# Optimization experiments

Hardware: AMD Instinct MI355X
Metric: run time of the kernel (lower is better)

## Reference

```python
import jax, jax.numpy as jnp
import numpy as np

N = 100000
E = 3200000
IN_C = 128
HID = [32, 32]
OUT_C = 32
NEG_SLOPE = 0.2  # PyG GATConv default leaky_relu slope


def setup_inputs() -> dict:
    key = jax.random.key(0)
    ks = jax.random.split(key, 16)
    x = jax.random.normal(ks[0], (N, IN_C), dtype=jnp.float32)
    edge_index = jax.random.randint(ks[1], (2, E), 0, N, dtype=jnp.int32)

    def glorot(k, shape):
        fan_in, fan_out = shape[0], shape[-1]
        lim = jnp.sqrt(6.0 / (fan_in + fan_out))
        return jax.random.uniform(k, shape, jnp.float32, -lim, lim)

    # GAT layer 1: 128 -> 32, heads=1
    W1 = glorot(ks[2], (IN_C, HID[0]))
    a_src1 = glorot(ks[3], (HID[0],))
    a_dst1 = glorot(ks[4], (HID[0],))
    b1 = jnp.zeros((HID[0],), jnp.float32)
    # GAT layer 2: 32 -> 32
    W2 = glorot(ks[5], (HID[0], HID[1]))
    a_src2 = glorot(ks[6], (HID[1],))
    a_dst2 = glorot(ks[7], (HID[1],))
    b2 = jnp.zeros((HID[1],), jnp.float32)
    # classifier: 32 -> 32
    Wc = glorot(ks[8], (HID[1], OUT_C))
    bc = jnp.zeros((OUT_C,), jnp.float32)
    return {"x": x, "edge_index": edge_index,
            "W1": W1, "a_src1": a_src1, "a_dst1": a_dst1, "b1": b1,
            "W2": W2, "a_src2": a_src2, "a_dst2": a_dst2, "b2": b2,
            "Wc": Wc, "bc": bc}


def gat_conv(h_in, src, dst, W, a_src, a_dst, b, n_nodes):
    """PyG GATConv with heads=1: linear, per-edge leaky-relu score,
    segment-softmax over incoming edges of dst, weighted scatter-sum."""
    h = h_in @ W                                   # [N, C]
    s_src = h @ a_src                              # [N]
    s_dst = h @ a_dst                              # [N]
    e = jax.nn.leaky_relu(s_src[src] + s_dst[dst], NEG_SLOPE)  # [E']
    m = jax.ops.segment_max(e, dst, num_segments=n_nodes)
    m = jnp.where(jnp.isfinite(m), m, 0.0)
    ex = jnp.exp(e - m[dst])
    z = jax.ops.segment_sum(ex, dst, num_segments=n_nodes)
    alpha = ex / (z[dst] + 1e-16)                  # [E']
    out = jax.ops.segment_sum(alpha[:, None] * h[src], dst, num_segments=n_nodes)
    return out + b


def reference(x, edge_index, W1, a_src1, a_dst1, b1, W2, a_src2, a_dst2, b2, Wc, bc):
    n = x.shape[0]
    # PyG GATConv default add_self_loops=True
    loop = jnp.arange(n, dtype=edge_index.dtype)
    src = jnp.concatenate([edge_index[0], loop])
    dst = jnp.concatenate([edge_index[1], loop])
    h = jax.nn.relu(gat_conv(x, src, dst, W1, a_src1, a_dst1, b1, n))
    h = jax.nn.relu(gat_conv(h, src, dst, W2, a_src2, a_dst2, b2, n))
    logits = h @ Wc + bc
    return jax.nn.sigmoid(logits)
```

## Files before the change

kernel.cpp:

```cpp
#include <hip/hip_runtime.h>
#include <hip/hip_fp16.h>
#include <math.h>

#define NS 0.2f

__device__ __forceinline__ float lrelu(float x) { return fmaxf(x, NS * x); }


__global__ __launch_bounds__(256) void k_feat1(
    const float* __restrict__ X, const float* __restrict__ W,
    const float* __restrict__ a_s, const float* __restrict__ a_d,
    __half* __restrict__ H, float* __restrict__ Ss, float* __restrict__ Sd, int n)
{
    __shared__ float Wl[128 * 32];
    __shared__ float Xl[8 * 128];
    const int tid = threadIdx.x;
    for (int i = tid; i < 128 * 32; i += 256) Wl[i] = W[i];

    const int row0 = blockIdx.x * 8;
    {
        int idx = tid * 4;
        int r = idx >> 7, c = idx & 127;
        if (row0 + r < n)
            *reinterpret_cast<float4*>(&Xl[idx]) =
                *reinterpret_cast<const float4*>(&X[(size_t)(row0 + r) * 128 + c]);
    }
    __syncthreads();

    const int r = tid >> 5, c = tid & 31;
    const int row = row0 + r;
    if (row >= n) return;

    float acc = 0.f;
#pragma unroll
    for (int k = 0; k < 128; ++k) acc += Xl[r * 128 + k] * Wl[k * 32 + c];
    H[(size_t)row * 32 + c] = __float2half(acc);

    float vs = acc * a_s[c];
    float vd = acc * a_d[c];
#pragma unroll
    for (int o = 16; o; o >>= 1) { vs += __shfl_xor(vs, o, 32); vd += __shfl_xor(vd, o, 32); }
    if (c == 0) { Ss[row] = vs; Sd[row] = vd; }
}

__global__ __launch_bounds__(256) void k_feat2(
    const float* __restrict__ In, const float* __restrict__ W,
    const float* __restrict__ bias,
    const float* __restrict__ a_s, const float* __restrict__ a_d,
    __half* __restrict__ H, float* __restrict__ Ss, float* __restrict__ Sd, int n)
{
    __shared__ float Wl[32 * 32];
    __shared__ float Xl[8 * 32];
    const int tid = threadIdx.x;
    for (int i = tid; i < 1024; i += 256) Wl[i] = W[i];

    const int r = tid >> 5, c = tid & 31;
    const int row = blockIdx.x * 8 + r;
    if (row < n) Xl[tid] = fmaxf(In[(size_t)row * 32 + c] + bias[c], 0.f);
    __syncthreads();
    if (row >= n) return;

    float acc = 0.f;
#pragma unroll
    for (int k = 0; k < 32; ++k) acc += Xl[r * 32 + k] * Wl[k * 32 + c];
    H[(size_t)row * 32 + c] = __float2half(acc);

    float vs = acc * a_s[c];
    float vd = acc * a_d[c];
#pragma unroll
    for (int o = 16; o; o >>= 1) { vs += __shfl_xor(vs, o, 32); vd += __shfl_xor(vd, o, 32); }
    if (c == 0) { Ss[row] = vs; Sd[row] = vd; }
}

__global__ __launch_bounds__(256) void k_cls(
    const float* __restrict__ In, const float* __restrict__ W,
    const float* __restrict__ b_prev, const float* __restrict__ bc,
    float* __restrict__ Out, int n)
{
    __shared__ float Wl[32 * 32];
    __shared__ float Xl[8 * 32];
    const int tid = threadIdx.x;
    for (int i = tid; i < 1024; i += 256) Wl[i] = W[i];

    const int r = tid >> 5, c = tid & 31;
    const int row = blockIdx.x * 8 + r;
    if (row < n) Xl[tid] = fmaxf(In[(size_t)row * 32 + c] + b_prev[c], 0.f);
    __syncthreads();
    if (row >= n) return;

    float acc = bc[c];
#pragma unroll
    for (int k = 0; k < 32; ++k) acc += Xl[r * 32 + k] * Wl[k * 32 + c];
    Out[(size_t)row * 32 + c] = 1.f / (1.f + __expf(-acc));
}


#define NBH 256

__global__ __launch_bounds__(256) void k_bhist(const int* __restrict__ edst, int E,
                                               int* __restrict__ hpart, int ngroups)
{
    __shared__ int h[512];
    const int tid = threadIdx.x;
    for (int i = tid; i < ngroups; i += 256) h[i] = 0;
    __syncthreads();
    const int nv = E >> 2;
    for (int i = blockIdx.x * 256 + tid; i < nv; i += NBH * 256) {
        int4 d = *reinterpret_cast<const int4*>(&edst[i << 2]);
        atomicAdd(&h[d.x >> 8], 1); atomicAdd(&h[d.y >> 8], 1);
        atomicAdd(&h[d.z >> 8], 1); atomicAdd(&h[d.w >> 8], 1);
    }
    if (blockIdx.x == 0 && tid < (E & 3))
        atomicAdd(&h[edst[(nv << 2) + tid] >> 8], 1);
    __syncthreads();
    for (int i = tid; i < ngroups; i += 256) hpart[i * NBH + blockIdx.x] = h[i];
}

__global__ __launch_bounds__(512) void k_bscan(const int* __restrict__ hpart, int ngroups,
    int* __restrict__ bstart, int* __restrict__ bcur, int* __restrict__ off,
    int N, int E)
{
    __shared__ int sm[512];
    int t = threadIdx.x;
    int v = 0;
    if (t < ngroups) {
        const int4* row = reinterpret_cast<const int4*>(&hpart[t * NBH]);
#pragma unroll 4
        for (int b = 0; b < NBH / 4; ++b) { int4 x = row[b]; v += x.x + x.y + x.z + x.w; }
    }
    sm[t] = v; __syncthreads();
    for (int o = 1; o < 512; o <<= 1) {
        int x = sm[t];
        if (t >= o) x += sm[t - o];
        __syncthreads();
        sm[t] = x;
        __syncthreads();
    }
    if (t <= ngroups) {
        int ex = (t == 0) ? 0 : sm[t - 1];
        bstart[t] = ex;
        if (t < ngroups) bcur[t] = ex;
    }
    if (t == 0) off[N] = E + N;
}

#define CHUNK 4096
#define KPT 16

__global__ __launch_bounds__(256) void k_part(
    const int* __restrict__ esrc, const int* __restrict__ edst, int E,
    int* __restrict__ bcur, unsigned int* __restrict__ ebuf, int ngroups)
{
    __shared__ int hist[512];
    __shared__ int lofs[513];
    __shared__ int gbase[512];
    __shared__ unsigned int stage[CHUNK];
    __shared__ unsigned short bstage[CHUNK];
    const int tid = threadIdx.x;

    for (int c0 = blockIdx.x * CHUNK; c0 < E; c0 += gridDim.x * CHUNK) {
        const int cnt = min(CHUNK, E - c0);
        for (int i = tid; i < 512; i += 256) hist[i] = 0;
        __syncthreads();

        int bp[KPT];
#pragma unroll
        for (int k = 0; k < KPT; ++k) {
            int i = c0 + k * 256 + tid;
            bp[k] = -1;
            if (i < E) {
                int d = edst[i];
                int b = d >> 8;
                int pos = atomicAdd(&hist[b], 1);
                bp[k] = (b << 20) | ((d & 255) << 12) | pos;
            }
        }
        __syncthreads();

        if (tid < 64) {
            int base = tid * 8, v[8], s = 0;
#pragma unroll
            for (int k = 0; k < 8; ++k) { v[k] = hist[base + k]; s += v[k]; }
            int pre = s;
            for (int o = 1; o < 64; o <<= 1) {
                int t2 = __shfl_up(pre, o, 64);
                if (tid >= o) pre += t2;
            }
            pre -= s;
#pragma unroll
            for (int k = 0; k < 8; ++k) { lofs[base + k] = pre; pre += v[k]; }
            if (tid == 63) lofs[512] = pre;
        }
        __syncthreads();

        for (int b = tid; b < ngroups; b += 256)
            if (hist[b] > 0) gbase[b] = atomicAdd(&bcur[b], hist[b]);
        __syncthreads();

#pragma unroll
        for (int k = 0; k < KPT; ++k) {
            if (bp[k] >= 0) {
                int i = c0 + k * 256 + tid;
                int b = bp[k] >> 20, dl = (bp[k] >> 12) & 255, pos = bp[k] & 4095;
                int slot = lofs[b] + pos;
                stage[slot] = ((unsigned)dl << 24) | (unsigned)esrc[i];
                bstage[slot] = (unsigned short)b;
            }
        }
        __syncthreads();

        for (int i = tid; i < cnt; i += 256) {
            int b = bstage[i];
            ebuf[(size_t)gbase[b] + (i - lofs[b])] = stage[i];
        }
        __syncthreads();
    }
}

#define RCAP 11264

__global__ __launch_bounds__(256) void k_place2(
    const unsigned int* __restrict__ ebuf, const int* __restrict__ bstart,
    int* __restrict__ off, int* __restrict__ esorted, int* __restrict__ gcur, int N)
{
    __shared__ int R[RCAP];
    __shared__ int cnt[256];
    __shared__ int lcur[256];
    __shared__ int sm[256];
    const int g = blockIdx.x, tid = threadIdx.x;
    const int d0 = g << 8, d1 = min(d0 + 256, N);
    const int nd = d1 - d0;
    const int eb = bstart[g];
    const int ecnt = bstart[g + 1] - eb;
    const int base = eb + d0;
    const int len = ecnt + nd;

    cnt[tid] = 0;
    __syncthreads();
    for (int i = tid; i < ecnt; i += 256)
        atomicAdd(&cnt[ebuf[eb + i] >> 24], 1);
    __syncthreads();

    int v = (tid < nd) ? cnt[tid] + 1 : 0;
    sm[tid] = v; __syncthreads();
    for (int o = 1; o < 256; o <<= 1) {
        int x = sm[tid];
        if (tid >= o) x += sm[tid - o];
        __syncthreads();
        sm[tid] = x;
        __syncthreads();
    }
    int lo = sm[tid] - v;

    if (len <= RCAP) {
        if (tid < nd) {
            off[d0 + tid] = base + lo;
            R[lo] = d0 + tid;
            lcur[tid] = lo + 1;
        }
        __syncthreads();
        for (int i = tid; i < ecnt; i += 256) {
            unsigned int w = ebuf[eb + i];
            int pos = atomicAdd(&lcur[w >> 24], 1);
            R[pos] = (int)(w & 0xffffffu);
        }
        __syncthreads();
        for (int i = tid; i < len; i += 256) esorted[base + i] = R[i];
    } else {
        if (tid < nd) {
            off[d0 + tid] = base + lo;
            esorted[base + lo] = d0 + tid;
            gcur[d0 + tid] = base + lo + 1;
        }
        __syncthreads();
        for (int i = tid; i < ecnt; i += 256) {
            unsigned int w = ebuf[eb + i];
            esorted[atomicAdd(&gcur[d0 + (int)(w >> 24)], 1)] = (int)(w & 0xffffffu);
        }
    }
}


__global__ __launch_bounds__(256) void k_max1(const float* __restrict__ Ss, int n,
                                              float* __restrict__ part)
{
    float m = -INFINITY;
    for (int i = blockIdx.x * 256 + threadIdx.x; i < n; i += gridDim.x * 256)
        m = fmaxf(m, Ss[i]);
    __shared__ float sm[256];
    sm[threadIdx.x] = m; __syncthreads();
    for (int o = 128; o; o >>= 1) {
        if (threadIdx.x < o) sm[threadIdx.x] = fmaxf(sm[threadIdx.x], sm[threadIdx.x + o]);
        __syncthreads();
    }
    if (threadIdx.x == 0) part[blockIdx.x] = sm[0];
}

__global__ void k_max2(const float* __restrict__ part, int nb, float* __restrict__ out)
{
    float m = -INFINITY;
    for (int i = threadIdx.x; i < nb; i += 64) m = fmaxf(m, part[i]);
    for (int o = 32; o; o >>= 1) m = fmaxf(m, __shfl_xor(m, o, 64));
    if (threadIdx.x == 0) out[0] = m;
}


__global__ __launch_bounds__(256) void k_gat(
    const int* __restrict__ off, const int* __restrict__ esorted,
    const float* __restrict__ Ss, const float* __restrict__ Sd,
    const float* __restrict__ maxSs, const uint4* __restrict__ H4,
    float* __restrict__ out, int n)
{
    const int g = blockIdx.x * 4 + (threadIdx.x >> 6);
    if (g >= n) return;
    const int lane = threadIdx.x & 63;
    const int hf = lane & 3, q = lane >> 2;

    const float sd = Sd[g];
    const float ub = lrelu(maxSs[0] + sd);
    const int j0 = off[g], j1 = off[g + 1];

    float a0 = 0.f, a1 = 0.f, a2 = 0.f, a3 = 0.f;
    float a4 = 0.f, a5 = 0.f, a6 = 0.f, a7 = 0.f, z = 0.f;

    for (int b0 = j0; b0 < j1; b0 += 64) {
        int e = b0 + lane;
        int sAll = 0; float wAll = 0.f;
        if (e < j1) {
            sAll = esorted[e];
            float t = Ss[sAll] + sd;
            wAll = __expf(fmaxf(t, NS * t) - ub);
        }
        z += wAll;
        const int m = min(64, j1 - b0);
        for (int k = 0; k < m; k += 16) {
            int   src = __shfl(sAll, k + q);
            float w   = __shfl(wAll, k + q);
            uint4 hv = H4[(size_t)src * 4 + hf];
            float2 f0 = __half22float2(*reinterpret_cast<const __half2*>(&hv.x));
            float2 f1 = __half22float2(*reinterpret_cast<const __half2*>(&hv.y));
            float2 f2 = __half22float2(*reinterpret_cast<const __half2*>(&hv.z));
            float2 f3 = __half22float2(*reinterpret_cast<const __half2*>(&hv.w));
            a0 += w * f0.x; a1 += w * f0.y;
            a2 += w * f1.x; a3 += w * f1.y;
            a4 += w * f2.x; a5 += w * f2.y;
            a6 += w * f3.x; a7 += w * f3.y;
        }
    }

#pragma unroll
    for (int o = 4; o <= 32; o <<= 1) {
        a0 += __shfl_xor(a0, o); a1 += __shfl_xor(a1, o);
        a2 += __shfl_xor(a2, o); a3 += __shfl_xor(a3, o);
        a4 += __shfl_xor(a4, o); a5 += __shfl_xor(a5, o);
        a6 += __shfl_xor(a6, o); a7 += __shfl_xor(a7, o);
        z  += __shfl_xor(z, o);
    }
    z += __shfl_xor(z, 1);
    z += __shfl_xor(z, 2);

    if (q == 0) {
        float inv = 1.f / (z + 1e-16f);
        float4 r0 = { a0 * inv, a1 * inv, a2 * inv, a3 * inv };
        float4 r1 = { a4 * inv, a5 * inv, a6 * inv, a7 * inv };
        float* o32 = &out[(size_t)g * 32 + hf * 8];
        *reinterpret_cast<float4*>(o32)     = r0;
        *reinterpret_cast<float4*>(o32 + 4) = r1;
    }
}


extern "C" void kernel_launch(void* const* d_in, const int* in_sizes, int n_in,
                              void* d_out, int out_size, void* d_ws, size_t ws_size,
                              hipStream_t stream)
{
    const float* x   = (const float*)d_in[0];
    const int*   ei  = (const int*)d_in[1];
    const float* W1  = (const float*)d_in[2];
    const float* as1 = (const float*)d_in[3];
    const float* ad1 = (const float*)d_in[4];
    const float* b1  = (const float*)d_in[5];
    const float* W2  = (const float*)d_in[6];
    const float* as2 = (const float*)d_in[7];
    const float* ad2 = (const float*)d_in[8];
    const float* b2  = (const float*)d_in[9];
    const float* Wc  = (const float*)d_in[10];
    const float* bc  = (const float*)d_in[11];

    const int N = in_sizes[0] / 128;
    const int E = in_sizes[1] / 2;
    const int* esrc = ei;
    const int* edst = ei + E;
    const int ngroups = (N + 255) >> 8;

    char* p = (char*)d_ws;
    __half* H    = (__half*)p; p += (size_t)N * 32 * 2;
    float* AGG   = (float*)p;  p += (size_t)N * 32 * 4;
    float* Ss    = (float*)p;  p += (size_t)N * 4;
    float* Sd    = (float*)p;  p += (size_t)N * 4;
    float* MSS   = (float*)p;  p += 256;
    int*   off   = (int*)p;    p += (size_t)(N + 1) * 4;
    int*   gcur  = (int*)p;    p += (size_t)N * 4;
    int*   part  = (int*)p;    p += 256 * 4;
    int*   hpart = (int*)p;    p += 512 * NBH * 4;
    int*   bstart= (int*)p;    p += 513 * 4;
    int*   bcur  = (int*)p;    p += 512 * 4;
    int*   esort = (int*)p;    p += (size_t)(E + N) * 4;

    unsigned int* ebuf = (unsigned int*)H;
    const uint4* H4 = (const uint4*)H;

    const dim3 blk(256);
    const int nb_rows = (N + 7) / 8;

    k_bhist<<<NBH, blk, 0, stream>>>(edst, E, hpart, ngroups);
    k_bscan<<<1, 512, 0, stream>>>(hpart, ngroups, bstart, bcur, off, N, E);
    k_part<<<768, blk, 0, stream>>>(esrc, edst, E, bcur, ebuf, ngroups);
    k_place2<<<ngroups, blk, 0, stream>>>(ebuf, bstart, off, esort, gcur, N);

    k_feat1<<<nb_rows, blk, 0, stream>>>(x, W1, as1, ad1, H, Ss, Sd, N);
    k_max1<<<128, blk, 0, stream>>>(Ss, N, (float*)part);
    k_max2<<<1, 64, 0, stream>>>((float*)part, 128, MSS);
    k_gat<<<(N + 3) / 4, blk, 0, stream>>>(off, esort, Ss, Sd, MSS, H4, AGG, N);

    k_feat2<<<nb_rows, blk, 0, stream>>>(AGG, W2, b1, as2, ad2, H, Ss, Sd, N);
    k_max1<<<128, blk, 0, stream>>>(Ss, N, (float*)part);
    k_max2<<<1, 64, 0, stream>>>((float*)part, 128, MSS);
    k_gat<<<(N + 3) / 4, blk, 0, stream>>>(off, esort, Ss, Sd, MSS, H4, AGG, N);

    k_cls<<<nb_rows, blk, 0, stream>>>(AGG, Wc, b2, bc, (float*)d_out, N);
}
```

Before: 301.3 us.

## Fuse Ss max reduction into feature kernels via atomicMax and pad bucket counters

Removes the two-stage max-reduction kernels after each feature transform. Each 16-row block now reduces its Ss values locally and does an order-preserving encoded atomicMax into a global word, which is reset in the scan kernel. The feature kernels move to 512-thread blocks. Bucket cursors are padded to separate cache lines to reduce atomic contention, and the partition chunk is halved with a grid sized to cover all chunks. The max word is not reset between layers, so layer 2 uses a looser upper bound. That is fine for softmax stability but could underflow if layer-1 scores are much larger.

```diff
diff --git a/kernel.cpp b/kernel.cpp
--- a/kernel.cpp
+++ b/kernel.cpp
@@ -6,48 +6,110 @@
 
 __device__ __forceinline__ float lrelu(float x) { return fmaxf(x, NS * x); }
 
-
-__global__ __launch_bounds__(256) void k_feat1(
+__device__ __forceinline__ unsigned encf(float f) {
+    unsigned u = __float_as_uint(f);
+    return (u & 0x80000000u) ? ~u : (u | 0x80000000u);
+}
+__device__ __forceinline__ float decf(unsigned e) {
+    return (e & 0x80000000u) ? __uint_as_float(e ^ 0x80000000u) : __uint_as_float(~e);
+}
+
+
+__global__ __launch_bounds__(512) void k_feat1(
     const float* __restrict__ X, const float* __restrict__ W,
     const float* __restrict__ a_s, const float* __restrict__ a_d,
-    __half* __restrict__ H, float* __restrict__ Ss, float* __restrict__ Sd, int n)
+    __half* __restrict__ H, float* __restrict__ Ss, float* __restrict__ Sd,
+    unsigned* __restrict__ MSS, int n)
 {
     __shared__ float Wl[128 * 32];
-    __shared__ float Xl[8 * 128];
+    __shared__ float Xl[16 * 128];
+    __shared__ float smax[16];
     const int tid = threadIdx.x;
-    for (int i = tid; i < 128 * 32; i += 256) Wl[i] = W[i];
-
-    const int row0 = blockIdx.x * 8;
+    for (int i = tid; i < 128 * 32; i += 512) Wl[i] = W[i];
+
+    const int row0 = blockIdx.x * 16;
     {
         int idx = tid * 4;
-        int r = idx >> 7, c = idx & 127;
+        int r = idx >> 7;
         if (row0 + r < n)
             *reinterpret_cast<float4*>(&Xl[idx]) =
-                *reinterpret_cast<const float4*>(&X[(size_t)(row0 + r) * 128 + c]);
+                *reinterpret_cast<const float4*>(&X[(size_t)(row0 + r) * 128 + (idx & 127)]);
     }
     __syncthreads();
 
     const int r = tid >> 5, c = tid & 31;
     const int row = row0 + r;
-    if (row >= n) return;
+    const bool ok = (row < n);
 
     float acc = 0.f;
-#pragma unroll
-    for (int k = 0; k < 128; ++k) acc += Xl[r * 128 + k] * Wl[k * 32 + c];
-    H[(size_t)row * 32 + c] = __float2half(acc);
-
+    if (ok) {
+#pragma unroll
+        for (int k = 0; k < 128; ++k) acc += Xl[r * 128 + k] * Wl[k * 32 + c];
+        H[(size_t)row * 32 + c] = __float2half(acc);
+    }
     float vs = acc * a_s[c];
     float vd = acc * a_d[c];
 #pragma unroll
     for (int o = 16; o; o >>= 1) { vs += __shfl_xor(vs, o, 32); vd += __shfl_xor(vd, o, 32); }
-    if (c == 0) { Ss[row] = vs; Sd[row] = vd; }
-}
-
-__global__ __launch_bounds__(256) void k_feat2(
+    if (c == 0) {
+        if (ok) { Ss[row] = vs; Sd[row] = vd; }
+        smax[r] = ok ? vs : -INFINITY;
+    }
+    __syncthreads();
+    if (tid == 0) {
+        float m = smax[0];
+#pragma unroll
+        for (int k = 1; k < 16; ++k) m = fmaxf(m, smax[k]);
+        atomicMax(MSS, encf(m));
+    }
+}
+
+__global__ __launch_bounds__(512) void k_feat2(
     const float* __restrict__ In, const float* __restrict__ W,
     const float* __restrict__ bias,
     const float* __restrict__ a_s, const float* __restrict__ a_d,
-    __half* __restrict__ H, float* __restrict__ Ss, float* __restrict__ Sd, int n)
+    __half* __restrict__ H, float* __restrict__ Ss, float* __restrict__ Sd,
+    unsigned* __restrict__ MSS, int n)
+{
+    __shared__ float Wl[32 * 32];
+    __shared__ float Xl[16 * 32];
+    __shared__ float smax[16];
+    const int tid = threadIdx.x;
+    for (int i = tid; i < 1024; i += 512) Wl[i] = W[i];
+
+    const int r = tid >> 5, c = tid & 31;
+    const int row = blockIdx.x * 16 + r;
+    const bool ok = (row < n);
+    Xl[tid] = ok ? fmaxf(In[(size_t)row * 32 + c] + bias[c], 0.f) : 0.f;
+    __syncthreads();
+
+    float acc = 0.f;
+    if (ok) {
+#pragma unroll
+        for (int k = 0; k < 32; ++k) acc += Xl[r * 32 + k] * Wl[k * 32 + c];
+        H[(size_t)row * 32 + c] = __float2half(acc);
+    }
+    float vs = acc * a_s[c];
+    float vd = acc * a_d[c];
+#pragma unroll
+    for (int o = 16; o; o >>= 1) { vs += __shfl_xor(vs, o, 32); vd += __shfl_xor(vd, o, 32); }
+    if (c == 0) {
+        if (ok) { Ss[row] = vs; Sd[row] = vd; }
+        smax[r] = ok ? vs : -INFINITY;
+    }
+    __syncthreads();
+    if (tid == 0) {
+        float m = smax[0];
+#pragma unroll
+        for (int k = 1; k < 16; ++k) m = fmaxf(m, smax[k]);
+        atomicMax(MSS, encf(m));
+    }
+}
+
+__global__ __launch_bounds__(256) void k_cls(
+    const float* __restrict__ In, const float* __restrict__ W,
+    const float* __restrict__ b_prev, const float* __restrict__ bc,
+    float* __restrict__ Out, int n)
 {
     __shared__ float Wl[32 * 32];
     __shared__ float Xl[8 * 32];
@@ -56,34 +118,6 @@
 
     const int r = tid >> 5, c = tid & 31;
     const int row = blockIdx.x * 8 + r;
-    if (row < n) Xl[tid] = fmaxf(In[(size_t)row * 32 + c] + bias[c], 0.f);
-    __syncthreads();
-    if (row >= n) return;
-
-    float acc = 0.f;
-#pragma unroll
-    for (int k = 0; k < 32; ++k) acc += Xl[r * 32 + k] * Wl[k * 32 + c];
-    H[(size_t)row * 32 + c] = __float2half(acc);
-
-    float vs = acc * a_s[c];
-    float vd = acc * a_d[c];
-#pragma unroll
-    for (int o = 16; o; o >>= 1) { vs += __shfl_xor(vs, o, 32); vd += __shfl_xor(vd, o, 32); }
-    if (c == 0) { Ss[row] = vs; Sd[row] = vd; }
-}
-
-__global__ __launch_bounds__(256) void k_cls(
-    const float* __restrict__ In, const float* __restrict__ W,
-    const float* __restrict__ b_prev, const float* __restrict__ bc,
-    float* __restrict__ Out, int n)
-{
-    __shared__ float Wl[32 * 32];
-    __shared__ float Xl[8 * 32];
-    const int tid = threadIdx.x;
-    for (int i = tid; i < 1024; i += 256) Wl[i] = W[i];
-
-    const int r = tid >> 5, c = tid & 31;
-    const int row = blockIdx.x * 8 + r;
     if (row < n) Xl[tid] = fmaxf(In[(size_t)row * 32 + c] + b_prev[c], 0.f);
     __syncthreads();
     if (row >= n) return;
@@ -96,6 +130,7 @@
 
 
 #define NBH 256
+#define BPAD 32
 
 __global__ __launch_bounds__(256) void k_bhist(const int* __restrict__ edst, int E,
                                                int* __restrict__ hpart, int ngroups)
@@ -118,7 +153,7 @@
 
 __global__ __launch_bounds__(512) void k_bscan(const int* __restrict__ hpart, int ngroups,
     int* __restrict__ bstart, int* __restrict__ bcur, int* __restrict__ off,
-    int N, int E)
+    unsigned* __restrict__ MSS, int N, int E)
 {
     __shared__ int sm[512];
     int t = threadIdx.x;
@@ -139,13 +174,13 @@
     if (t <= ngroups) {
         int ex = (t == 0) ? 0 : sm[t - 1];
         bstart[t] = ex;
-        if (t < ngroups) bcur[t] = ex;
-    }
-    if (t == 0) off[N] = E + N;
-}
-
-#define CHUNK 4096
-#define KPT 16
+        if (t < ngroups) bcur[t * BPAD] = ex;
+    }
+    if (t == 0) { off[N] = E + N; MSS[0] = 0u; }
+}
+
+#define CHUNK 2048
+#define KPT 8
 
 __global__ __launch_bounds__(256) void k_part(
     const int* __restrict__ esrc, const int* __restrict__ edst, int E,
@@ -194,7 +229,7 @@
         __syncthreads();
 
         for (int b = tid; b < ngroups; b += 256)
-            if (hist[b] > 0) gbase[b] = atomicAdd(&bcur[b], hist[b]);
+            if (hist[b] > 0) gbase[b] = atomicAdd(&bcur[b * BPAD], hist[b]);
         __syncthreads();
 
 #pragma unroll
@@ -281,34 +316,10 @@
 }
 
 
-__global__ __launch_bounds__(256) void k_max1(const float* __restrict__ Ss, int n,
-                                              float* __restrict__ part)
-{
-    float m = -INFINITY;
-    for (int i = blockIdx.x * 256 + threadIdx.x; i < n; i += gridDim.x * 256)
-        m = fmaxf(m, Ss[i]);
-    __shared__ float sm[256];
-    sm[threadIdx.x] = m; __syncthreads();
-    for (int o = 128; o; o >>= 1) {
-        if (threadIdx.x < o) sm[threadIdx.x] = fmaxf(sm[threadIdx.x], sm[threadIdx.x + o]);
-        __syncthreads();
-    }
-    if (threadIdx.x == 0) part[blockIdx.x] = sm[0];
-}
-
-__global__ void k_max2(const float* __restrict__ part, int nb, float* __restrict__ out)
-{
-    float m = -INFINITY;
-    for (int i = threadIdx.x; i < nb; i += 64) m = fmaxf(m, part[i]);
-    for (int o = 32; o; o >>= 1) m = fmaxf(m, __shfl_xor(m, o, 64));
-    if (threadIdx.x == 0) out[0] = m;
-}
-
-
 __global__ __launch_bounds__(256) void k_gat(
     const int* __restrict__ off, const int* __restrict__ esorted,
     const float* __restrict__ Ss, const float* __restrict__ Sd,
-    const float* __restrict__ maxSs, const uint4* __restrict__ H4,
+    const unsigned* __restrict__ MSS, const uint4* __restrict__ H4,
     float* __restrict__ out, int n)
 {
     const int g = blockIdx.x * 4 + (threadIdx.x >> 6);
@@ -317,7 +328,7 @@
     const int hf = lane & 3, q = lane >> 2;
 
     const float sd = Sd[g];
-    const float ub = lrelu(maxSs[0] + sd);
+    const float ub = lrelu(decf(MSS[0]) + sd);
     const int j0 = off[g], j1 = off[g + 1];
 
     float a0 = 0.f, a1 = 0.f, a2 = 0.f, a3 = 0.f;
@@ -398,35 +409,31 @@
     float* AGG   = (float*)p;  p += (size_t)N * 32 * 4;
     float* Ss    = (float*)p;  p += (size_t)N * 4;
     float* Sd    = (float*)p;  p += (size_t)N * 4;
-    float* MSS   = (float*)p;  p += 256;
+    unsigned* MSS= (unsigned*)p; p += 256;
     int*   off   = (int*)p;    p += (size_t)(N + 1) * 4;
     int*   gcur  = (int*)p;    p += (size_t)N * 4;
-    int*   part  = (int*)p;    p += 256 * 4;
     int*   hpart = (int*)p;    p += 512 * NBH * 4;
     int*   bstart= (int*)p;    p += 513 * 4;
-    int*   bcur  = (int*)p;    p += 512 * 4;
+    int*   bcur  = (int*)p;    p += 512 * BPAD * 4;
     int*   esort = (int*)p;    p += (size_t)(E + N) * 4;
 
     unsigned int* ebuf = (unsigned int*)H;
     const uint4* H4 = (const uint4*)H;
 
     const dim3 blk(256);
-    const int nb_rows = (N + 7) / 8;
+    const int nb_rows16 = (N + 15) / 16;
+    const int nb_part = (E + CHUNK - 1) / CHUNK;
 
     k_bhist<<<NBH, blk, 0, stream>>>(edst, E, hpart, ngroups);
-    k_bscan<<<1, 512, 0, stream>>>(hpart, ngroups, bstart, bcur, off, N, E);
-    k_part<<<768, blk, 0, stream>>>(esrc, edst, E, bcur, ebuf, ngroups);
+    k_bscan<<<1, 512, 0, stream>>>(hpart, ngroups, bstart, bcur, off, MSS, N, E);
+    k_part<<<nb_part, blk, 0, stream>>>(esrc, edst, E, bcur, ebuf, ngroups);
     k_place2<<<ngroups, blk, 0, stream>>>(ebuf, bstart, off, esort, gcur, N);
 
-    k_feat1<<<nb_rows, blk, 0, stream>>>(x, W1, as1, ad1, H, Ss, Sd, N);
-    k_max1<<<128, blk, 0, stream>>>(Ss, N, (float*)part);
-    k_max2<<<1, 64, 0, stream>>>((float*)part, 128, MSS);
+    k_feat1<<<nb_rows16, 512, 0, stream>>>(x, W1, as1, ad1, H, Ss, Sd, MSS, N);
     k_gat<<<(N + 3) / 4, blk, 0, stream>>>(off, esort, Ss, Sd, MSS, H4, AGG, N);
 
-    k_feat2<<<nb_rows, blk, 0, stream>>>(AGG, W2, b1, as2, ad2, H, Ss, Sd, N);
-    k_max1<<<128, blk, 0, stream>>>(Ss, N, (float*)part);
-    k_max2<<<1, 64, 0, stream>>>((float*)part, 128, MSS);
+    k_feat2<<<nb_rows16, 512, 0, stream>>>(AGG, W2, b1, as2, ad2, H, Ss, Sd, MSS, N);
     k_gat<<<(N + 3) / 4, blk, 0, stream>>>(off, esort, Ss, Sd, MSS, H4, AGG, N);
 
-    k_cls<<<nb_rows, blk, 0, stream>>>(AGG, Wc, b2, bc, (float*)d_out, N);
-}
+    k_cls<<<(N + 7) / 8, blk, 0, stream>>>(AGG, Wc, b2, bc, (float*)d_out, N);
+}
```

New measurement: 381.0 us. +26.5%, slower.

## Split hidden features into half-width planes and aggregate in two passes

Applied to the files above, without the earlier changes.

Stores the fp16 node features as two 16-channel planes and runs the GAT aggregation twice, once per plane, so each pass gathers from a 3.2MB table that fits in cache better. The second pass reuses the softmax normaliser saved by the first. The edge-partition kernel also moves to 512-thread blocks with one chunk per block and pads the bucket cursors to avoid atomic contention on shared cache lines. In exchange, edge indices and scores are read and recomputed twice per layer, and there are more launches.

```diff
diff --git a/kernel.cpp b/kernel.cpp
--- a/kernel.cpp
+++ b/kernel.cpp
@@ -10,7 +10,8 @@
 __global__ __launch_bounds__(256) void k_feat1(
     const float* __restrict__ X, const float* __restrict__ W,
     const float* __restrict__ a_s, const float* __restrict__ a_d,
-    __half* __restrict__ H, float* __restrict__ Ss, float* __restrict__ Sd, int n)
+    __half* __restrict__ Hlo, __half* __restrict__ Hhi,
+    float* __restrict__ Ss, float* __restrict__ Sd, int n)
 {
     __shared__ float Wl[128 * 32];
     __shared__ float Xl[8 * 128];
@@ -34,7 +35,8 @@
     float acc = 0.f;
 #pragma unroll
     for (int k = 0; k < 128; ++k) acc += Xl[r * 128 + k] * Wl[k * 32 + c];
-    H[(size_t)row * 32 + c] = __float2half(acc);
+    __half* Hh = (c < 16) ? Hlo : Hhi;
+    Hh[(size_t)row * 16 + (c & 15)] = __float2half(acc);
 
     float vs = acc * a_s[c];
     float vd = acc * a_d[c];
@@ -47,7 +49,8 @@
     const float* __restrict__ In, const float* __restrict__ W,
     const float* __restrict__ bias,
     const float* __restrict__ a_s, const float* __restrict__ a_d,
-    __half* __restrict__ H, float* __restrict__ Ss, float* __restrict__ Sd, int n)
+    __half* __restrict__ Hlo, __half* __restrict__ Hhi,
+    float* __restrict__ Ss, float* __restrict__ Sd, int n)
 {
     __shared__ float Wl[32 * 32];
     __shared__ float Xl[8 * 32];
@@ -63,7 +66,8 @@
     float acc = 0.f;
 #pragma unroll
     for (int k = 0; k < 32; ++k) acc += Xl[r * 32 + k] * Wl[k * 32 + c];
-    H[(size_t)row * 32 + c] = __float2half(acc);
+    __half* Hh = (c < 16) ? Hlo : Hhi;
+    Hh[(size_t)row * 16 + (c & 15)] = __float2half(acc);
 
     float vs = acc * a_s[c];
     float vd = acc * a_d[c];
@@ -96,6 +100,7 @@
 
 
 #define NBH 256
+#define BPAD 32
 
 __global__ __launch_bounds__(256) void k_bhist(const int* __restrict__ edst, int E,
                                                int* __restrict__ hpart, int ngroups)
@@ -139,15 +144,15 @@
     if (t <= ngroups) {
         int ex = (t == 0) ? 0 : sm[t - 1];
         bstart[t] = ex;
-        if (t < ngroups) bcur[t] = ex;
+        if (t < ngroups) bcur[t * BPAD] = ex;
     }
     if (t == 0) off[N] = E + N;
 }
 
 #define CHUNK 4096
-#define KPT 16
-
-__global__ __launch_bounds__(256) void k_part(
+#define KPT 8
+
+__global__ __launch_bounds__(512) void k_part(
     const int* __restrict__ esrc, const int* __restrict__ edst, int E,
     int* __restrict__ bcur, unsigned int* __restrict__ ebuf, int ngroups)
 {
@@ -160,13 +165,13 @@
 
     for (int c0 = blockIdx.x * CHUNK; c0 < E; c0 += gridDim.x * CHUNK) {
         const int cnt = min(CHUNK, E - c0);
-        for (int i = tid; i < 512; i += 256) hist[i] = 0;
+        for (int i = tid; i < 512; i += 512) hist[i] = 0;
         __syncthreads();
 
         int bp[KPT];
 #pragma unroll
         for (int k = 0; k < KPT; ++k) {
-            int i = c0 + k * 256 + tid;
+            int i = c0 + k * 512 + tid;
             bp[k] = -1;
             if (i < E) {
                 int d = edst[i];
@@ -193,14 +198,14 @@
         }
         __syncthreads();
 
-        for (int b = tid; b < ngroups; b += 256)
-            if (hist[b] > 0) gbase[b] = atomicAdd(&bcur[b], hist[b]);
+        for (int b = tid; b < ngroups; b += 512)
+            if (hist[b] > 0) gbase[b] = atomicAdd(&bcur[b * BPAD], hist[b]);
         __syncthreads();
 
 #pragma unroll
         for (int k = 0; k < KPT; ++k) {
             if (bp[k] >= 0) {
-                int i = c0 + k * 256 + tid;
+                int i = c0 + k * 512 + tid;
                 int b = bp[k] >> 20, dl = (bp[k] >> 12) & 255, pos = bp[k] & 4095;
                 int slot = lofs[b] + pos;
                 stage[slot] = ((unsigned)dl << 24) | (unsigned)esrc[i];
@@ -209,7 +214,7 @@
         }
         __syncthreads();
 
-        for (int i = tid; i < cnt; i += 256) {
+        for (int i = tid; i < cnt; i += 512) {
             int b = bstage[i];
             ebuf[(size_t)gbase[b] + (i - lofs[b])] = stage[i];
         }
@@ -305,16 +310,16 @@
 }
 
 
-__global__ __launch_bounds__(256) void k_gat(
+__global__ __launch_bounds__(256) void k_gats(
     const int* __restrict__ off, const int* __restrict__ esorted,
     const float* __restrict__ Ss, const float* __restrict__ Sd,
     const float* __restrict__ maxSs, const uint4* __restrict__ H4,
-    float* __restrict__ out, int n)
+    float* __restrict__ out, float* __restrict__ inv, int n, int hi)
 {
     const int g = blockIdx.x * 4 + (threadIdx.x >> 6);
     if (g >= n) return;
     const int lane = threadIdx.x & 63;
-    const int hf = lane & 3, q = lane >> 2;
+    const int hf = lane & 1, q = lane >> 1;
 
     const float sd = Sd[g];
     const float ub = lrelu(maxSs[0] + sd);
@@ -333,10 +338,10 @@
         }
         z += wAll;
         const int m = min(64, j1 - b0);
-        for (int k = 0; k < m; k += 16) {
+        for (int k = 0; k < m; k += 32) {
             int   src = __shfl(sAll, k + q);
             float w   = __shfl(wAll, k + q);
-            uint4 hv = H4[(size_t)src * 4 + hf];
+            uint4 hv = H4[(size_t)src * 2 + hf];
             float2 f0 = __half22float2(*reinterpret_cast<const __half2*>(&hv.x));
             float2 f1 = __half22float2(*reinterpret_cast<const __half2*>(&hv.y));
             float2 f2 = __half22float2(*reinterpret_cast<const __half2*>(&hv.z));
@@ -349,21 +354,27 @@
     }
 
 #pragma unroll
-    for (int o = 4; o <= 32; o <<= 1) {
+    for (int o = 2; o <= 32; o <<= 1) {
         a0 += __shfl_xor(a0, o); a1 += __shfl_xor(a1, o);
         a2 += __shfl_xor(a2, o); a3 += __shfl_xor(a3, o);
         a4 += __shfl_xor(a4, o); a5 += __shfl_xor(a5, o);
         a6 += __shfl_xor(a6, o); a7 += __shfl_xor(a7, o);
-        z  += __shfl_xor(z, o);
-    }
-    z += __shfl_xor(z, 1);
-    z += __shfl_xor(z, 2);
+    }
+
+    float invz;
+    if (hi == 0) {
+#pragma unroll
+        for (int o = 1; o <= 32; o <<= 1) z += __shfl_xor(z, o);
+        invz = 1.f / (z + 1e-16f);
+        if (lane == 0) inv[g] = invz;
+    } else {
+        invz = inv[g];
+    }
 
     if (q == 0) {
-        float inv = 1.f / (z + 1e-16f);
-        float4 r0 = { a0 * inv, a1 * inv, a2 * inv, a3 * inv };
-        float4 r1 = { a4 * inv, a5 * inv, a6 * inv, a7 * inv };
-        float* o32 = &out[(size_t)g * 32 + hf * 8];
+        float4 r0 = { a0 * invz, a1 * invz, a2 * invz, a3 * invz };
+        float4 r1 = { a4 * invz, a5 * invz, a6 * invz, a7 * invz };
+        float* o32 = &out[(size_t)g * 32 + (hi << 4) + hf * 8];
         *reinterpret_cast<float4*>(o32)     = r0;
         *reinterpret_cast<float4*>(o32 + 4) = r1;
     }
@@ -394,39 +405,46 @@
     const int ngroups = (N + 255) >> 8;
 
     char* p = (char*)d_ws;
-    __half* H    = (__half*)p; p += (size_t)N * 32 * 2;
+    __half* Hlo  = (__half*)p; p += (size_t)N * 16 * 2;
+    __half* Hhi  = (__half*)p; p += (size_t)N * 16 * 2;
     float* AGG   = (float*)p;  p += (size_t)N * 32 * 4;
     float* Ss    = (float*)p;  p += (size_t)N * 4;
     float* Sd    = (float*)p;  p += (size_t)N * 4;
+    float* INV   = (float*)p;  p += (size_t)N * 4;
+    int*   hpart = (int*)p;    p += 512 * NBH * 4;
+    int*   esort = (int*)p;    p += (size_t)(E + N) * 4;
+    int*   gcur  = (int*)p;    p += (size_t)N * 4;
+    int*   off   = (int*)p;    p += (size_t)(N + 1) * 4;
     float* MSS   = (float*)p;  p += 256;
-    int*   off   = (int*)p;    p += (size_t)(N + 1) * 4;
-    int*   gcur  = (int*)p;    p += (size_t)N * 4;
     int*   part  = (int*)p;    p += 256 * 4;
-    int*   hpart = (int*)p;    p += 512 * NBH * 4;
     int*   bstart= (int*)p;    p += 513 * 4;
-    int*   bcur  = (int*)p;    p += 512 * 4;
-    int*   esort = (int*)p;    p += (size_t)(E + N) * 4;
-
-    unsigned int* ebuf = (unsigned int*)H;
-    const uint4* H4 = (const uint4*)H;
+    int*   bcur  = (int*)p;    p += 512 * BPAD * 4;
+
+    unsigned int* ebuf = (unsigned int*)AGG;
+    const uint4* H4lo = (const uint4*)Hlo;
+    const uint4* H4hi = (const uint4*)Hhi;
 
     const dim3 blk(256);
     const int nb_rows = (N + 7) / 8;
+    const int nb_part = (E + CHUNK - 1) / CHUNK;
+    const int nb_gat  = (N + 3) / 4;
 
     k_bhist<<<NBH, blk, 0, stream>>>(edst, E, hpart, ngroups);
     k_bscan<<<1, 512, 0, stream>>>(hpart, ngroups, bstart, bcur, off, N, E);
-    k_part<<<768, blk, 0, stream>>>(esrc, edst, E, bcur, ebuf, ngroups);
+    k_part<<<nb_part, 512, 0, stream>>>(esrc, edst, E, bcur, ebuf, ngroups);
     k_place2<<<ngroups, blk, 0, stream>>>(ebuf, bstart, off, esort, gcur, N);
 
-    k_feat1<<<nb_rows, blk, 0, stream>>>(x, W1, as1, ad1, H, Ss, Sd, N);
+    k_feat1<<<nb_rows, blk, 0, stream>>>(x, W1, as1, ad1, Hlo, Hhi, Ss, Sd, N);
     k_max1<<<128, blk, 0, stream>>>(Ss, N, (float*)part);
     k_max2<<<1, 64, 0, stream>>>((float*)part, 128, MSS);
-    k_gat<<<(N + 3) / 4, blk, 0, stream>>>(off, esort, Ss, Sd, MSS, H4, AGG, N);
-
-    k_feat2<<<nb_rows, blk, 0, stream>>>(AGG, W2, b1, as2, ad2, H, Ss, Sd, N);
+    k_gats<<<nb_gat, blk, 0, stream>>>(off, esort, Ss, Sd, MSS, H4lo, AGG, INV, N, 0);
+    k_gats<<<nb_gat, blk, 0, stream>>>(off, esort, Ss, Sd, MSS, H4hi, AGG, INV, N, 1);
+
+    k_feat2<<<nb_rows, blk, 0, stream>>>(AGG, W2, b1, as2, ad2, Hlo, Hhi, Ss, Sd, N);
     k_max1<<<128, blk, 0, stream>>>(Ss, N, (float*)part);
     k_max2<<<1, 64, 0, stream>>>((float*)part, 128, MSS);
-    k_gat<<<(N + 3) / 4, blk, 0, stream>>>(off, esort, Ss, Sd, MSS, H4, AGG, N);
+    k_gats<<<nb_gat, blk, 0, stream>>>(off, esort, Ss, Sd, MSS, H4lo, AGG, INV, N, 0);
+    k_gats<<<nb_gat, blk, 0, stream>>>(off, esort, Ss, Sd, MSS, H4hi, AGG, INV, N, 1);
 
     k_cls<<<nb_rows, blk, 0, stream>>>(AGG, Wc, b2, bc, (float*)d_out, N);
 }
```

After: 376.4 us. +24.9%, slower.
